# Optimization experiments

Hardware: AMD Instinct MI355X
Metric: run time of the kernel (lower is better)

The kernel has to match this reference:

```python
import jax, jax.numpy as jnp
import numpy as np

N = 2048
IN_FEAT = 256
OUT_FEAT = 64
E_FEAT = 32
NHID = 64
ALPHA = 0.2
NHEADS = 4
NLAYERS = 3
NEG_INF = -9e15


def setup_inputs() -> dict:
    key = jax.random.key(0)
    ks = jax.random.split(key, 6)
    x = jax.random.normal(ks[0], (N, IN_FEAT), dtype=jnp.float32)
    adj = jax.random.randint(ks[1], (N, N), 0, 2, dtype=jnp.int32)
    e = jax.random.normal(ks[2], (N, N, E_FEAT), dtype=jnp.float32)
    # All layers share shapes because in_feat == nhid*nheads and out_feat == nhid.
    # xavier-ish scale
    W_e = jax.random.normal(ks[3], (NLAYERS, NHEADS, E_FEAT, IN_FEAT), dtype=jnp.float32) * (1.414 * (2.0 / (E_FEAT + IN_FEAT)) ** 0.5)
    W = jax.random.normal(ks[4], (NLAYERS, NHEADS, IN_FEAT, NHID), dtype=jnp.float32) * (1.414 * (2.0 / (IN_FEAT + NHID)) ** 0.5)
    a = jax.random.normal(ks[5], (NLAYERS, NHEADS, 3 * NHID), dtype=jnp.float32) * (1.414 * (2.0 / (3 * NHID + 1)) ** 0.5)
    return {"x": x, "adj": adj, "e": e, "W_e": W_e, "W": W, "a": a}


def reference(x, adj, e, W_e, W, a):
    # dropout = 0.0 / eval mode -> identity
    out = W.shape[-1]
    nlayers = W.shape[0]
    mask = (adj > 0)[None]  # [1, N, N], broadcast over heads
    for l in range(nlayers):
        islast = (l == nlayers - 1)
        h = jnp.einsum('ni,hio->hno', x, W[l])  # [H, N, out]
        a1 = a[l, :, :out]            # [H, out]
        a2 = a[l, :, out:2 * out]     # [H, out]
        a3 = a[l, :, 2 * out:]        # [H, out]
        # score_ij = leakyrelu(a1.h_i + a2.h_j + a3.(e_ij @ W_e @ W))
        coef = jnp.einsum('heo,ho->he', jnp.einsum('hei,hio->heo', W_e[l], W[l]), a3)  # [H, E_FEAT]
        e_score = jnp.einsum('nmf,hf->hnm', e, coef)  # [H, N, N]
        s1 = jnp.einsum('hno,ho->hn', h, a1)[:, :, None]
        s2 = jnp.einsum('hno,ho->hn', h, a2)[:, None, :]
        score = jax.nn.leaky_relu(s1 + s2 + e_score, ALPHA)
        att = jax.nn.softmax(jnp.where(mask, score, NEG_INF), axis=-1)
        h_prime = jnp.einsum('hnm,hmo->hno', att, h)  # [H, N, out]
        if islast:
            x = jax.nn.elu(h_prime.mean(axis=0))  # [N, out]
        else:
            # concat heads along feature dim (head-major), with per-head elu
            x = jnp.transpose(jax.nn.elu(h_prime), (1, 0, 2)).reshape(h_prime.shape[1], -1)
    return x
```

## Files before the change

kernel.cpp:

```cpp
#include <hip/hip_runtime.h>
#include <cstdint>
#include <cstddef>

#define Nn 2048
#define FIN 256
#define EFEAT 32
#define HID 64
#define NH 4
#define NL 3
#define LRELU_A 0.2f

typedef _Float16 h4 __attribute__((ext_vector_type(4)));
typedef _Float16 h8 __attribute__((ext_vector_type(8)));
typedef float f4 __attribute__((ext_vector_type(4)));

#define NEGH ((_Float16)(-60000.0f))

__global__ void k_coef(const float* __restrict__ W, const float* __restrict__ We,
                       const float* __restrict__ a, float* __restrict__ coef) {
  int lh = blockIdx.x;
  int t = threadIdx.x;
  __shared__ float tl[FIN];
  const float* Wb = W + (size_t)lh * FIN * HID;
  const float* ab = a + (size_t)lh * (3 * HID) + 2 * HID;
  float acc = 0.f;
#pragma unroll 8
  for (int o = 0; o < HID; ++o) acc = fmaf(Wb[(size_t)t * HID + o], ab[o], acc);
  tl[t] = acc;
  __syncthreads();
  if (t < EFEAT) {
    const float* Web = We + ((size_t)lh * EFEAT + t) * FIN;
    float c = 0.f;
    for (int i = 0; i < FIN; ++i) c = fmaf(Web[i], tl[i], c);
    coef[lh * EFEAT + t] = c;
  }
}

template <int C>
__global__ __launch_bounds__(256) void k_escore(
    const float* __restrict__ e, const int* __restrict__ adj,
    const float* __restrict__ coef, _Float16* __restrict__ es) {
  size_t idx = (size_t)blockIdx.x * 256 + threadIdx.x;
  int m = (int)(idx & (Nn - 1));
  int n = (int)(idx >> 11);
  int mt = m >> 6, ml = m & 63;
  const size_t cstride = (size_t)32 * Nn * 64;
  size_t sbase = ((size_t)mt * Nn + n) * 64 + (size_t)ml;
  int aj = adj[idx];
  float evv[EFEAT] = {};
  if (aj != 0) {
    const float4* ep = (const float4*)(e + idx * EFEAT);
#pragma unroll
    for (int g = 0; g < 8; ++g) {
      float4 v = ep[g];
      evv[g * 4 + 0] = v.x; evv[g * 4 + 1] = v.y; evv[g * 4 + 2] = v.z; evv[g * 4 + 3] = v.w;
    }
  }
#pragma clang loop unroll(disable)
  for (int c = 0; c < C; ++c) {
    const float* cf = coef + c * EFEAT;
    float acc = 0.f;
#pragma unroll
    for (int f = 0; f < EFEAT; ++f) acc = fmaf(evv[f], cf[f], acc);
    es[(size_t)c * cstride + sbase] = aj ? (_Float16)acc : NEGH;
  }
}

__global__ __launch_bounds__(256) void k_h(
    const float* __restrict__ x, const float* __restrict__ W,
    const float* __restrict__ a, int layer,
    _Float16* __restrict__ hT, float* __restrict__ s1, float* __restrict__ s2) {
  int t = threadIdx.x;
  int n0 = blockIdx.x * 4;
  int h = t >> 6, o = t & 63;
  const float* Wb = W + ((size_t)(layer * NH + h) * FIN) * HID + o;
  const float* xb = x + (size_t)n0 * FIN;
  float acc[4] = {};
  for (int i0 = 0; i0 < FIN; i0 += 4) {
    float w0 = Wb[(size_t)(i0 + 0) * HID];
    float w1 = Wb[(size_t)(i0 + 1) * HID];
    float w2 = Wb[(size_t)(i0 + 2) * HID];
    float w3 = Wb[(size_t)(i0 + 3) * HID];
#pragma unroll
    for (int j = 0; j < 4; ++j) {
      float4 xv = *(const float4*)(xb + (size_t)j * FIN + i0);
      acc[j] = fmaf(xv.x, w0, acc[j]);
      acc[j] = fmaf(xv.y, w1, acc[j]);
      acc[j] = fmaf(xv.z, w2, acc[j]);
      acc[j] = fmaf(xv.w, w3, acc[j]);
    }
  }
  const float* ab = a + (size_t)(layer * NH + h) * (3 * HID);
  float a1v = ab[o], a2v = ab[HID + o];
#pragma unroll
  for (int j = 0; j < 4; ++j) {
    float r1 = acc[j] * a1v, r2 = acc[j] * a2v;
#pragma unroll
    for (int d = 1; d < 64; d <<= 1) {
      r1 += __shfl_xor(r1, d, 64);
      r2 += __shfl_xor(r2, d, 64);
    }
    if (o == 0) { s1[h * Nn + n0 + j] = r1; s2[h * Nn + n0 + j] = r2; }
  }
  int mt = n0 >> 6, ml = n0 & 63;
  h4 hv;
#pragma unroll
  for (int j = 0; j < 4; ++j) hv[j] = (_Float16)acc[j];
  *(h4*)(hT + (((size_t)h * 32 + mt) * 64 + o) * 64 + ml) = hv;
}

__global__ __launch_bounds__(512, 2) void k_attn(
    const _Float16* __restrict__ es, const _Float16* __restrict__ hT,
    const float* __restrict__ s1, const float* __restrict__ s2,
    float* __restrict__ hp, float* __restrict__ xn, int layer, int last) {
  int h = blockIdx.x;
  int n0 = blockIdx.y * 16;
  int t = threadIdx.x;
  int w = t >> 6;
  int l = t & 63;
  int col = l & 15, grp = l >> 4;
  int n = n0 + col;
  float s1v = s1[h * Nn + n];
  const _Float16* esb = es + (size_t)(layer * NH + h) * ((size_t)32 * Nn * 64);
  const _Float16* hTb = hT + (size_t)h * ((size_t)32 * 64 * 64);
  const float* s2b = s2 + h * Nn;

  h4 sc16[16];
  float pmax = -3.0e38f;
#pragma unroll
  for (int c16 = 0; c16 < 16; ++c16) {
    int m0 = w * 256 + c16 * 16;
    int mt = m0 >> 6;
    int ml0 = (m0 & 63) + grp * 4;
    h4 ev = *(const h4*)(esb + ((size_t)mt * Nn + n) * 64 + ml0);
    float4 sv = *(const float4*)(s2b + m0 + grp * 4);
    float sc0 = s1v + sv.x + (float)ev[0]; sc0 = fmaxf(sc0, LRELU_A * sc0);
    float sc1 = s1v + sv.y + (float)ev[1]; sc1 = fmaxf(sc1, LRELU_A * sc1);
    float sc2 = s1v + sv.z + (float)ev[2]; sc2 = fmaxf(sc2, LRELU_A * sc2);
    float sc3 = s1v + sv.w + (float)ev[3]; sc3 = fmaxf(sc3, LRELU_A * sc3);
    h4 sch;
    sch[0] = (_Float16)sc0; sch[1] = (_Float16)sc1;
    sch[2] = (_Float16)sc2; sch[3] = (_Float16)sc3;
    sc16[c16] = sch;
    pmax = fmaxf(pmax, fmaxf(fmaxf(sc0, sc1), fmaxf(sc2, sc3)));
  }
  pmax = fmaxf(pmax, __shfl_xor(pmax, 16, 64));
  float M = fmaxf(pmax, __shfl_xor(pmax, 32, 64));

  float S = 0.f;
  f4 acc[4] = {};
#pragma unroll
  for (int c16 = 0; c16 < 16; ++c16) {
    int m0 = w * 256 + c16 * 16;
    int mt = m0 >> 6;
    int ml0 = (m0 & 63) + grp * 4;
    h4 scv = sc16[c16];
    float p0 = __expf((float)scv[0] - M);
    float p1 = __expf((float)scv[1] - M);
    float p2 = __expf((float)scv[2] - M);
    float p3 = __expf((float)scv[3] - M);
    S += p0 + p1 + p2 + p3;
    h4 pb;
    pb[0] = (_Float16)p0; pb[1] = (_Float16)p1;
    pb[2] = (_Float16)p2; pb[3] = (_Float16)p3;
    const _Float16* hp0 = hTb + ((size_t)mt * 64 + col) * 64 + ml0;
#pragma unroll
    for (int ot = 0; ot < 4; ++ot) {
      h4 af = *(const h4*)(hp0 + (size_t)ot * 16 * 64);
      acc[ot] = __builtin_amdgcn_mfma_f32_16x16x16f16(af, pb, acc[ot], 0, 0, 0);
    }
  }
  S += __shfl_xor(S, 16, 64);
  S += __shfl_xor(S, 32, 64);

  __shared__ float red[8][16][64];
  __shared__ float Mw[8][16];
  __shared__ float Sw[8][16];
  if (l < 16) { Mw[w][l] = M; Sw[w][l] = S; }
#pragma unroll
  for (int ot = 0; ot < 4; ++ot)
    *(f4*)&red[w][col][ot * 16 + grp * 4] = acc[ot];
  __syncthreads();

  if (t < 256) {
    int nl = t >> 4, o0 = (t & 15) * 4;
    float Ms = Mw[0][nl];
#pragma unroll
    for (int ww = 1; ww < 8; ++ww) Ms = fmaxf(Ms, Mw[ww][nl]);
    float Ssum = 0.f;
    f4 v = {};
#pragma unroll
    for (int ww = 0; ww < 8; ++ww) {
      float f = __expf(Mw[ww][nl] - Ms);
      Ssum = fmaf(Sw[ww][nl], f, Ssum);
      f4 r = *(const f4*)&red[ww][nl][o0];
      v += r * f;
    }
    float is = 1.0f / Ssum;
    v *= is;
    if (last) {
      *(f4*)(hp + ((size_t)h * Nn + n0 + nl) * HID + o0) = v;
    } else {
      f4 xo;
#pragma unroll
      for (int k = 0; k < 4; ++k) xo[k] = v[k] > 0.f ? v[k] : expm1f(v[k]);
      *(f4*)(xn + (size_t)(n0 + nl) * FIN + h * HID + o0) = xo;
    }
  }
}

__global__ void k_out(const float* __restrict__ hp, float* __restrict__ out) {
  int idx = blockIdx.x * 256 + threadIdx.x;
  int n = idx >> 6, o = idx & 63;
  size_t b = (size_t)n * HID + o;
  float v = 0.25f * (hp[b] + hp[(size_t)Nn * HID + b] +
                     hp[2 * (size_t)Nn * HID + b] + hp[3 * (size_t)Nn * HID + b]);
  out[idx] = v > 0.f ? v : expm1f(v);
}

extern "C" void kernel_launch(void* const* d_in, const int* in_sizes, int n_in,
                              void* d_out, int out_size, void* d_ws, size_t ws_size,
                              hipStream_t stream) {
  const float* x_in = (const float*)d_in[0];
  const int* adj = (const int*)d_in[1];
  const float* e = (const float*)d_in[2];
  const float* We = (const float*)d_in[3];
  const float* W = (const float*)d_in[4];
  const float* a = (const float*)d_in[5];
  float* out = (float*)d_out;

  char* ws = (char*)d_ws;
  size_t off = 0;
  auto alloc = [&](size_t bytes) -> void* {
    off = (off + 255) & ~(size_t)255;
    void* p = ws + off;
    off += bytes;
    return p;
  };
  float* coef = (float*)alloc((size_t)NL * NH * EFEAT * sizeof(float));
  float* s1 = (float*)alloc((size_t)NH * Nn * sizeof(float));
  float* s2 = (float*)alloc((size_t)NH * Nn * sizeof(float));
  float* hp = (float*)alloc((size_t)NH * Nn * HID * sizeof(float));
  float* xA = (float*)alloc((size_t)Nn * FIN * sizeof(float));
  float* xB = (float*)alloc((size_t)Nn * FIN * sizeof(float));
  _Float16* hT = (_Float16*)alloc((size_t)NH * 32 * 64 * 64 * sizeof(_Float16));
  _Float16* es = (_Float16*)alloc((size_t)NL * NH * 32 * Nn * 64 * sizeof(_Float16));

  hipLaunchKernelGGL(k_coef, dim3(NL * NH), dim3(256), 0, stream, W, We, a, coef);

  size_t total = (size_t)Nn * Nn;
  hipLaunchKernelGGL((k_escore<NL * NH>), dim3((unsigned)(total / 256)), dim3(256), 0, stream,
                     e, adj, coef, es);

  for (int l = 0; l < NL; ++l) {
    const float* xcur = (l == 0) ? x_in : ((l == 1) ? xA : xB);
    float* xn = (l == 0) ? xA : xB;
    hipLaunchKernelGGL(k_h, dim3(Nn / 4), dim3(256), 0, stream, xcur, W, a, l, hT, s1, s2);
    hipLaunchKernelGGL(k_attn, dim3(NH, Nn / 16), dim3(512), 0, stream,
                       es, hT, s1, s2, hp, xn, l, l == NL - 1 ? 1 : 0);
  }
  hipLaunchKernelGGL(k_out, dim3(Nn * HID / 256), dim3(256), 0, stream, hp, out);
}
```

Baseline: 259.6 us.

## Fuse all stages into one persistent cooperative kernel with grid-wide syncs

Wraps the coef, escore, per-layer h/attention and output stages in device functions and runs them from a single cooperative megakernel of 512 blocks, with grid.sync between dependent stages. The aim is to remove the nine separate kernel launches and the gaps between them. The old multi-kernel path stays as a fallback if the cooperative launch fails. In exchange, __launch_bounds__(512,4) tightens the register budget of the attention body, which may cause spills. The escore stage also loses the latency hiding it got from a large grid, and each grid barrier adds its own cost.

Result: slower. 1.018 ms (+291.9%).

```diff
diff --git a/kernel.cpp b/kernel.cpp
--- a/kernel.cpp
+++ b/kernel.cpp
@@ -1,6 +1,9 @@
 #include <hip/hip_runtime.h>
+#include <hip/hip_cooperative_groups.h>
 #include <cstdint>
 #include <cstddef>
+
+namespace cg = cooperative_groups;
 
 #define Nn 2048
 #define FIN 256
@@ -11,22 +14,22 @@
 #define LRELU_A 0.2f
 
 typedef _Float16 h4 __attribute__((ext_vector_type(4)));
-typedef _Float16 h8 __attribute__((ext_vector_type(8)));
 typedef float f4 __attribute__((ext_vector_type(4)));
 
 #define NEGH ((_Float16)(-60000.0f))
 
-__global__ void k_coef(const float* __restrict__ W, const float* __restrict__ We,
-                       const float* __restrict__ a, float* __restrict__ coef) {
-  int lh = blockIdx.x;
-  int t = threadIdx.x;
-  __shared__ float tl[FIN];
+
+__device__ __forceinline__ void coef_body(int lh, int t, const float* __restrict__ W,
+                                          const float* __restrict__ We, const float* __restrict__ a,
+                                          float* __restrict__ coef, float* tl) {
   const float* Wb = W + (size_t)lh * FIN * HID;
   const float* ab = a + (size_t)lh * (3 * HID) + 2 * HID;
-  float acc = 0.f;
+  if (t < FIN) {
+    float acc = 0.f;
 #pragma unroll 8
-  for (int o = 0; o < HID; ++o) acc = fmaf(Wb[(size_t)t * HID + o], ab[o], acc);
-  tl[t] = acc;
+    for (int o = 0; o < HID; ++o) acc = fmaf(Wb[(size_t)t * HID + o], ab[o], acc);
+    tl[t] = acc;
+  }
   __syncthreads();
   if (t < EFEAT) {
     const float* Web = We + ((size_t)lh * EFEAT + t) * FIN;
@@ -36,11 +39,10 @@
   }
 }
 
-template <int C>
-__global__ __launch_bounds__(256) void k_escore(
-    const float* __restrict__ e, const int* __restrict__ adj,
-    const float* __restrict__ coef, _Float16* __restrict__ es) {
-  size_t idx = (size_t)blockIdx.x * 256 + threadIdx.x;
+__device__ __forceinline__ void escore_body(size_t idx, const float* __restrict__ e,
+                                            const int* __restrict__ adj,
+                                            const float* __restrict__ coef,
+                                            _Float16* __restrict__ es) {
   int m = (int)(idx & (Nn - 1));
   int n = (int)(idx >> 11);
   int mt = m >> 6, ml = m & 63;
@@ -57,7 +59,7 @@
     }
   }
 #pragma clang loop unroll(disable)
-  for (int c = 0; c < C; ++c) {
+  for (int c = 0; c < NL * NH; ++c) {
     const float* cf = coef + c * EFEAT;
     float acc = 0.f;
 #pragma unroll
@@ -66,12 +68,10 @@
   }
 }
 
-__global__ __launch_bounds__(256) void k_h(
-    const float* __restrict__ x, const float* __restrict__ W,
-    const float* __restrict__ a, int layer,
-    _Float16* __restrict__ hT, float* __restrict__ s1, float* __restrict__ s2) {
-  int t = threadIdx.x;
-  int n0 = blockIdx.x * 4;
+__device__ __forceinline__ void h_body(int n0, int t, const float* __restrict__ x,
+                                       const float* __restrict__ W, const float* __restrict__ a,
+                                       int layer, _Float16* __restrict__ hT,
+                                       float* __restrict__ s1, float* __restrict__ s2) {
   int h = t >> 6, o = t & 63;
   const float* Wb = W + ((size_t)(layer * NH + h) * FIN) * HID + o;
   const float* xb = x + (size_t)n0 * FIN;
@@ -109,13 +109,14 @@
   *(h4*)(hT + (((size_t)h * 32 + mt) * 64 + o) * 64 + ml) = hv;
 }
 
-__global__ __launch_bounds__(512, 2) void k_attn(
-    const _Float16* __restrict__ es, const _Float16* __restrict__ hT,
-    const float* __restrict__ s1, const float* __restrict__ s2,
-    float* __restrict__ hp, float* __restrict__ xn, int layer, int last) {
-  int h = blockIdx.x;
-  int n0 = blockIdx.y * 16;
-  int t = threadIdx.x;
+__device__ __forceinline__ void attn_body(int h, int n0, int t,
+                                          const _Float16* __restrict__ es,
+                                          const _Float16* __restrict__ hT,
+                                          const float* __restrict__ s1,
+                                          const float* __restrict__ s2,
+                                          float* __restrict__ hp, float* __restrict__ xn,
+                                          int layer, int last,
+                                          float (*red)[16][64], float (*Mw)[16], float (*Sw)[16]) {
   int w = t >> 6;
   int l = t & 63;
   int col = l & 15, grp = l >> 4;
@@ -173,9 +174,6 @@
   S += __shfl_xor(S, 16, 64);
   S += __shfl_xor(S, 32, 64);
 
-  __shared__ float red[8][16][64];
-  __shared__ float Mw[8][16];
-  __shared__ float Sw[8][16];
   if (l < 16) { Mw[w][l] = M; Sw[w][l] = S; }
 #pragma unroll
   for (int ot = 0; ot < 4; ++ot)
@@ -207,6 +205,82 @@
       *(f4*)(xn + (size_t)(n0 + nl) * FIN + h * HID + o0) = xo;
     }
   }
+  __syncthreads();
+}
+
+__global__ __launch_bounds__(512, 4) void k_mega(
+    const float* __restrict__ x_in, const int* __restrict__ adj, const float* __restrict__ e,
+    const float* __restrict__ We, const float* __restrict__ W, const float* __restrict__ a,
+    float* __restrict__ out, float* __restrict__ coef, float* __restrict__ s1,
+    float* __restrict__ s2, float* __restrict__ hp, float* __restrict__ xA,
+    float* __restrict__ xB, _Float16* __restrict__ hT, _Float16* __restrict__ es) {
+  cg::grid_group grid = cg::this_grid();
+  __shared__ float red[8][16][64];
+  __shared__ float Mw[8][16];
+  __shared__ float Sw[8][16];
+  __shared__ float tl[FIN];
+  int bid = blockIdx.x;
+  int t = threadIdx.x;
+
+  if (bid < NL * NH) coef_body(bid, t, W, We, a, coef, tl);
+  grid.sync();
+
+#pragma clang loop unroll(disable)
+  for (int it = 0; it < 16; ++it) {
+    size_t idx = ((size_t)bid * 16 + it) * 512 + t;
+    escore_body(idx, e, adj, coef, es);
+  }
+  grid.sync();
+
+  for (int l = 0; l < NL; ++l) {
+    const float* xcur = (l == 0) ? x_in : ((l == 1) ? xA : xB);
+    float* xn = (l == 0) ? xA : xB;
+    if (t < 256) h_body(bid * 4, t, xcur, W, a, l, hT, s1, s2);
+    grid.sync();
+    attn_body(bid >> 7, (bid & 127) * 16, t, es, hT, s1, s2, hp, xn, l,
+              (l == NL - 1) ? 1 : 0, red, Mw, Sw);
+    grid.sync();
+  }
+
+  int i = bid * 512 + t;
+  if (i < Nn * HID) {
+    int n = i >> 6, o = i & 63;
+    size_t b = (size_t)n * HID + o;
+    float v = 0.25f * (hp[b] + hp[(size_t)Nn * HID + b] +
+                       hp[2 * (size_t)Nn * HID + b] + hp[3 * (size_t)Nn * HID + b]);
+    out[i] = v > 0.f ? v : expm1f(v);
+  }
+}
+
+__global__ void k_coef(const float* __restrict__ W, const float* __restrict__ We,
+                       const float* __restrict__ a, float* __restrict__ coef) {
+  __shared__ float tl[FIN];
+  coef_body(blockIdx.x, threadIdx.x, W, We, a, coef, tl);
+}
+
+__global__ __launch_bounds__(256) void k_escore(
+    const float* __restrict__ e, const int* __restrict__ adj,
+    const float* __restrict__ coef, _Float16* __restrict__ es) {
+  size_t idx = (size_t)blockIdx.x * 256 + threadIdx.x;
+  escore_body(idx, e, adj, coef, es);
+}
+
+__global__ __launch_bounds__(256) void k_h(
+    const float* __restrict__ x, const float* __restrict__ W,
+    const float* __restrict__ a, int layer,
+    _Float16* __restrict__ hT, float* __restrict__ s1, float* __restrict__ s2) {
+  h_body(blockIdx.x * 4, threadIdx.x, x, W, a, layer, hT, s1, s2);
+}
+
+__global__ __launch_bounds__(512, 2) void k_attn(
+    const _Float16* __restrict__ es, const _Float16* __restrict__ hT,
+    const float* __restrict__ s1, const float* __restrict__ s2,
+    float* __restrict__ hp, float* __restrict__ xn, int layer, int last) {
+  __shared__ float red[8][16][64];
+  __shared__ float Mw[8][16];
+  __shared__ float Sw[8][16];
+  attn_body(blockIdx.x, blockIdx.y * 16, threadIdx.x, es, hT, s1, s2, hp, xn, layer, last,
+            red, Mw, Sw);
 }
 
 __global__ void k_out(const float* __restrict__ hp, float* __restrict__ out) {
@@ -246,12 +320,17 @@
   _Float16* hT = (_Float16*)alloc((size_t)NH * 32 * 64 * 64 * sizeof(_Float16));
   _Float16* es = (_Float16*)alloc((size_t)NL * NH * 32 * Nn * 64 * sizeof(_Float16));
 
+  void* args[] = {(void*)&x_in, (void*)&adj, (void*)&e, (void*)&We, (void*)&W, (void*)&a,
+                  (void*)&out, (void*)&coef, (void*)&s1, (void*)&s2, (void*)&hp,
+                  (void*)&xA, (void*)&xB, (void*)&hT, (void*)&es};
+  hipError_t err = hipLaunchCooperativeKernel((void*)k_mega, dim3(512), dim3(512),
+                                              args, 0, stream);
+  if (err == hipSuccess) return;
+
   hipLaunchKernelGGL(k_coef, dim3(NL * NH), dim3(256), 0, stream, W, We, a, coef);
-
   size_t total = (size_t)Nn * Nn;
-  hipLaunchKernelGGL((k_escore<NL * NH>), dim3((unsigned)(total / 256)), dim3(256), 0, stream,
+  hipLaunchKernelGGL(k_escore, dim3((unsigned)(total / 256)), dim3(256), 0, stream,
                      e, adj, coef, es);
-
   for (int l = 0; l < NL; ++l) {
     const float* xcur = (l == 0) ? x_in : ((l == 1) ? xA : xB);
     float* xn = (l == 0) ? xA : xB;
```

## Fuse edge-score and layer-0 projection into one kernel, vectorize edge-score per thread

Applied to the files above, without the earlier changes.

The edge-score kernel is rewritten so each thread handles 8 consecutive columns of a row. It loads the adjacency as int4, computes all 12 layer-head dot products with packed float2 math and writes 16-byte half8 stores instead of scalar half stores. The layer-0 h projection is merged into the same launch as extra blocks, removing one launch and the serialization between them. The per-thread register footprint grows (12 h8 accumulators plus 16 f2), which may reduce occupancy on this bandwidth-bound pass over the 512MB edge tensor.

New measurement: 467.8 us. 1.8x slower.

```diff
diff --git a/kernel.cpp b/kernel.cpp
--- a/kernel.cpp
+++ b/kernel.cpp
@@ -12,6 +12,7 @@
 
 typedef _Float16 h4 __attribute__((ext_vector_type(4)));
 typedef _Float16 h8 __attribute__((ext_vector_type(8)));
+typedef float f2 __attribute__((ext_vector_type(2)));
 typedef float f4 __attribute__((ext_vector_type(4)));
 
 #define NEGH ((_Float16)(-60000.0f))
@@ -36,42 +37,52 @@
   }
 }
 
-template <int C>
-__global__ __launch_bounds__(256) void k_escore(
-    const float* __restrict__ e, const int* __restrict__ adj,
-    const float* __restrict__ coef, _Float16* __restrict__ es) {
-  size_t idx = (size_t)blockIdx.x * 256 + threadIdx.x;
-  int m = (int)(idx & (Nn - 1));
-  int n = (int)(idx >> 11);
-  int mt = m >> 6, ml = m & 63;
+__device__ __forceinline__ void escore_row(int n, int t, const float* __restrict__ e,
+                                           const int* __restrict__ adj,
+                                           const float* __restrict__ coef,
+                                           _Float16* __restrict__ es) {
+  int m8 = t * 8;
+  size_t rowm = (size_t)n * Nn + m8;
+  const int4* ap = (const int4*)(adj + rowm);
+  int4 aj0 = ap[0], aj1 = ap[1];
+  int ajv[8] = {aj0.x, aj0.y, aj0.z, aj0.w, aj1.x, aj1.y, aj1.z, aj1.w};
+  h8 sc[NL * NH];
+#pragma unroll
+  for (int mi = 0; mi < 8; ++mi) {
+    f2 ev[16];
+#pragma unroll
+    for (int g = 0; g < 16; ++g) ev[g] = (f2){0.f, 0.f};
+    if (ajv[mi] != 0) {
+      const f4* ep = (const f4*)(e + (rowm + mi) * EFEAT);
+#pragma unroll
+      for (int g = 0; g < 8; ++g) {
+        f4 v = ep[g];
+        ev[2 * g + 0][0] = v[0]; ev[2 * g + 0][1] = v[1];
+        ev[2 * g + 1][0] = v[2]; ev[2 * g + 1][1] = v[3];
+      }
+    }
+#pragma unroll
+    for (int c = 0; c < NL * NH; ++c) {
+      const f2* cf = (const f2*)(coef + c * EFEAT);
+      f2 a2 = {0.f, 0.f};
+#pragma unroll
+      for (int f = 0; f < 16; ++f) a2 += ev[f] * cf[f];
+      float r = a2[0] + a2[1];
+      sc[c][mi] = ajv[mi] ? (_Float16)r : NEGH;
+    }
+  }
+  int mt = m8 >> 6, ml0 = m8 & 63;
   const size_t cstride = (size_t)32 * Nn * 64;
-  size_t sbase = ((size_t)mt * Nn + n) * 64 + (size_t)ml;
-  int aj = adj[idx];
-  float evv[EFEAT] = {};
-  if (aj != 0) {
-    const float4* ep = (const float4*)(e + idx * EFEAT);
-#pragma unroll
-    for (int g = 0; g < 8; ++g) {
-      float4 v = ep[g];
-      evv[g * 4 + 0] = v.x; evv[g * 4 + 1] = v.y; evv[g * 4 + 2] = v.z; evv[g * 4 + 3] = v.w;
-    }
-  }
-#pragma clang loop unroll(disable)
-  for (int c = 0; c < C; ++c) {
-    const float* cf = coef + c * EFEAT;
-    float acc = 0.f;
-#pragma unroll
-    for (int f = 0; f < EFEAT; ++f) acc = fmaf(evv[f], cf[f], acc);
-    es[(size_t)c * cstride + sbase] = aj ? (_Float16)acc : NEGH;
-  }
-}
-
-__global__ __launch_bounds__(256) void k_h(
-    const float* __restrict__ x, const float* __restrict__ W,
-    const float* __restrict__ a, int layer,
-    _Float16* __restrict__ hT, float* __restrict__ s1, float* __restrict__ s2) {
-  int t = threadIdx.x;
-  int n0 = blockIdx.x * 4;
+  _Float16* dst = es + ((size_t)mt * Nn + n) * 64 + ml0;
+#pragma unroll
+  for (int c = 0; c < NL * NH; ++c)
+    *(h8*)(dst + (size_t)c * cstride) = sc[c];
+}
+
+__device__ __forceinline__ void h_body(int n0, int t, const float* __restrict__ x,
+                                       const float* __restrict__ W, const float* __restrict__ a,
+                                       int layer, _Float16* __restrict__ hT,
+                                       float* __restrict__ s1, float* __restrict__ s2) {
   int h = t >> 6, o = t & 63;
   const float* Wb = W + ((size_t)(layer * NH + h) * FIN) * HID + o;
   const float* xb = x + (size_t)n0 * FIN;
@@ -107,6 +118,26 @@
 #pragma unroll
   for (int j = 0; j < 4; ++j) hv[j] = (_Float16)acc[j];
   *(h4*)(hT + (((size_t)h * 32 + mt) * 64 + o) * 64 + ml) = hv;
+}
+
+__global__ __launch_bounds__(256) void k_mega(
+    const float* __restrict__ e, const int* __restrict__ adj, const float* __restrict__ coef,
+    _Float16* __restrict__ es, const float* __restrict__ x, const float* __restrict__ W,
+    const float* __restrict__ a, _Float16* __restrict__ hT,
+    float* __restrict__ s1, float* __restrict__ s2) {
+  int bid = blockIdx.x;
+  if (bid < Nn) {
+    escore_row(bid, threadIdx.x, e, adj, coef, es);
+  } else {
+    h_body((bid - Nn) * 4, threadIdx.x, x, W, a, 0, hT, s1, s2);
+  }
+}
+
+__global__ __launch_bounds__(256) void k_h(
+    const float* __restrict__ x, const float* __restrict__ W,
+    const float* __restrict__ a, int layer,
+    _Float16* __restrict__ hT, float* __restrict__ s1, float* __restrict__ s2) {
+  h_body(blockIdx.x * 4, threadIdx.x, x, W, a, layer, hT, s1, s2);
 }
 
 __global__ __launch_bounds__(512, 2) void k_attn(
@@ -247,15 +278,15 @@
   _Float16* es = (_Float16*)alloc((size_t)NL * NH * 32 * Nn * 64 * sizeof(_Float16));
 
   hipLaunchKernelGGL(k_coef, dim3(NL * NH), dim3(256), 0, stream, W, We, a, coef);
-
-  size_t total = (size_t)Nn * Nn;
-  hipLaunchKernelGGL((k_escore<NL * NH>), dim3((unsigned)(total / 256)), dim3(256), 0, stream,
-                     e, adj, coef, es);
+  hipLaunchKernelGGL(k_mega, dim3(Nn + Nn / 4), dim3(256), 0, stream,
+                     e, adj, coef, es, x_in, W, a, hT, s1, s2);
 
   for (int l = 0; l < NL; ++l) {
-    const float* xcur = (l == 0) ? x_in : ((l == 1) ? xA : xB);
+    if (l > 0) {
+      const float* xcur = (l == 1) ? xA : xB;
+      hipLaunchKernelGGL(k_h, dim3(Nn / 4), dim3(256), 0, stream, xcur, W, a, l, hT, s1, s2);
+    }
     float* xn = (l == 0) ? xA : xB;
-    hipLaunchKernelGGL(k_h, dim3(Nn / 4), dim3(256), 0, stream, xcur, W, a, l, hT, s1, s2);
     hipLaunchKernelGGL(k_attn, dim3(NH, Nn / 16), dim3(512), 0, stream,
                        es, hT, s1, s2, hp, xn, l, l == NL - 1 ? 1 : 0);
   }
```
